# Kernel tuning notes

Hardware: AMD Instinct MI355X
Metric: run time of the kernel (lower is better)

## Reference

```python
import jax, jax.numpy as jnp
import numpy as np

B, H, A, D = 4096, 50, 32, 64          # batch, history len, neighbor count, embed_dim
NU, NV = 100000, 100000                # num users, num items
L = H + A                              # total gathered entries per node


def setup_inputs() -> dict:
    key = jax.random.key(0)
    ks = jax.random.split(key, 16)
    # embedding tables (u2e/v2e uniform(-1,1) as in module init, r2e ~ N(0,1) default)
    u2e = jax.random.uniform(ks[0], (NU, D), minval=-1.0, maxval=1.0, dtype=jnp.float32)
    v2e = jax.random.uniform(ks[1], (NV, D), minval=-1.0, maxval=1.0, dtype=jnp.float32)
    r2e = jax.random.normal(ks[2], (7, D), dtype=jnp.float32)
    relation_att = jax.random.normal(ks[3], (2 * D,), dtype=jnp.float32)
    s = 1.0 / np.sqrt(2 * D)  # torch Linear default init bound
    agg_W = jax.random.uniform(ks[4], (D, 2 * D), minval=-s, maxval=s, dtype=jnp.float32)
    agg_b = jax.random.uniform(ks[5], (D,), minval=-s, maxval=s, dtype=jnp.float32)
    lin1_W = jax.random.uniform(ks[6], (D, 2 * D), minval=-s, maxval=s, dtype=jnp.float32)
    lin1_b = jax.random.uniform(ks[7], (D,), minval=-s, maxval=s, dtype=jnp.float32)
    nodes_u = jax.random.randint(ks[8], (B,), 0, NU)
    nodes_v = jax.random.randint(ks[9], (B,), 0, NV)
    hist_u = jax.random.randint(ks[10], (B, H), 0, NV)   # user history = items
    hist_ur = jax.random.randint(ks[11], (B, H), 0, 6)   # ratings 0..5
    adj_u = jax.random.randint(ks[12], (B, A), 0, NU)    # social neighbors = users
    hist_v = jax.random.randint(ks[13], (B, H), 0, NU)   # item history = users
    hist_vr = jax.random.randint(ks[14], (B, H), 0, 6)
    adj_v = jax.random.randint(ks[15], (B, A), 0, NV)    # item-adj neighbors = items
    return dict(u2e=u2e, v2e=v2e, r2e=r2e, relation_att=relation_att,
                agg_W=agg_W, agg_b=agg_b, lin1_W=lin1_W, lin1_b=lin1_b,
                nodes_u=nodes_u, nodes_v=nodes_v,
                hist_u=hist_u, hist_ur=hist_ur, adj_u=adj_u,
                hist_v=hist_v, hist_vr=hist_vr, adj_v=adj_v)


def _encode(node_tab, target_tab, hist_tab, neigh_tab, r2e, relation_att,
            agg_W, agg_b, lin1_W, lin1_b, nodes, targets, hn, hr, adj):
    # Node_Encoder.forward + Node_Aggregator (percent=1.0 -> deterministic:
    # multinomial selects all indices; softmax-weighted sum is permutation-invariant).
    nf = node_tab[nodes]                                   # [B, D]
    tf = target_tab[targets]                               # [B, D]
    # query (computed as in original; with percent=1 the norm-softmax sampling
    # probability does not affect the output)
    _q = jnp.concatenate([nf, tf], axis=-1) @ agg_W.T + agg_b  # [B, D]
    hist_feat = jnp.concatenate([hist_tab[hn], neigh_tab[adj]], axis=1)  # [B, L, D]
    rates = jnp.concatenate([hr, jnp.full(adj.shape, 6, dtype=hr.dtype)], axis=1)
    rate_feat = r2e[rates]                                 # [B, L, D]
    sel = jnp.concatenate([hist_feat, rate_feat], axis=-1)  # [B, L, 2D]
    logits = jnp.einsum('ble,e->bl', sel, relation_att)    # [B, L]
    p = jax.nn.softmax(logits, axis=1)                     # softmax2 over entries
    neigh = jnp.einsum('bl,bld->bd', p, hist_feat)         # weighted sum [B, D]
    comb = jnp.concatenate([nf, neigh], axis=-1)           # [B, 2D]
    return jax.nn.relu(comb @ lin1_W.T + lin1_b)           # [B, D]


def reference(u2e, v2e, r2e, relation_att, agg_W, agg_b, lin1_W, lin1_b,
              nodes_u, nodes_v, hist_u, hist_ur, adj_u, hist_v, hist_vr, adj_v):
    # user side: isitem=False -> node=u2e, target=v2e, hist=v2e, neighbor=u2e
    eu = _encode(u2e, v2e, v2e, u2e, r2e, relation_att, agg_W, agg_b, lin1_W, lin1_b,
                 nodes_u, nodes_v, hist_u, hist_ur, adj_u)
    # item side: isitem=True -> node=v2e, target=u2e, hist=u2e, neighbor=v2e
    ev = _encode(v2e, u2e, u2e, v2e, r2e, relation_att, agg_W, agg_b, lin1_W, lin1_b,
                 nodes_v, nodes_u, hist_v, hist_vr, adj_v)
    return jnp.sum(eu * ev, axis=1)                        # [B]
```

## Files before the change

kernel.cpp:

```cpp
#include <hip/hip_runtime.h>


#define NB 4096
#define NH 50
#define NA 32
#define ND 64

__global__ __launch_bounds__(256, 4) void graphconsis_main(
    const float* __restrict__ u2e, const float* __restrict__ v2e,
    const float* __restrict__ r2e, const float* __restrict__ ra,
    const float* __restrict__ lin1_W, const float* __restrict__ lin1_b,
    const int* __restrict__ nodes_u, const int* __restrict__ nodes_v,
    const int* __restrict__ hist_u, const int* __restrict__ hist_ur,
    const int* __restrict__ adj_u,
    const int* __restrict__ hist_v, const int* __restrict__ hist_vr,
    const int* __restrict__ adj_v,
    float* __restrict__ out)
{
    __shared__ float lds_comb[4][128];
    __shared__ float ed[4][64];

    const int wid  = threadIdx.x >> 6;
    const int lane = threadIdx.x & 63;
    const int g    = lane >> 4;
    const int j    = lane & 15;
    const int side = wid >> 1;
    const int b    = __builtin_amdgcn_readfirstlane(blockIdx.x * 2 + (wid & 1));

    const float* nodeTab  = side ? v2e : u2e;
    const float* histTab  = side ? u2e : v2e;
    const float* neighTab = side ? v2e : u2e;
    const int* nodes = side ? nodes_v : nodes_u;
    const int* hn    = side ? hist_v  : hist_u;
    const int* hr    = side ? hist_vr : hist_ur;
    const int* adj   = side ? adj_v   : adj_u;

    const float4 ra4 = *(const float4*)(ra + 4 * j);

    const int lcl  = (lane < NH) ? lane : NH - 1;
    const int hraw = hn[b * NH + lcl];
    const int rraw = hr[b * NH + lcl];
    const int araw = adj[b * NA + (lane & 31)];

    int hidx[13];
    #pragma unroll
    for (int k = 0; k < 13; ++k) {
        int l = 4 * k + g; if (l > NH - 1) l = NH - 1;
        hidx[k] = __shfl(hraw, l);
    }
    int aidx[8];
    #pragma unroll
    for (int k = 0; k < 8; ++k)
        aidx[k] = __shfl(araw, 4 * k + g);
    const int hrv = __shfl(rraw, (4 * j + g < NH) ? (4 * j + g) : NH - 1);
    const bool hrv_valid = (4 * j + g) < NH;

    const float4 nf4 = *(const float4*)(nodeTab + nodes[b] * ND + 4 * j);
    float4 rh[13];
    #pragma unroll
    for (int k = 0; k < 13; ++k)
        rh[k] = *(const float4*)(histTab + hidx[k] * ND + 4 * j);
    float4 raj[8];
    #pragma unroll
    for (int k = 0; k < 8; ++k)
        raj[k] = *(const float4*)(neighTab + aidx[k] * ND + 4 * j);

    const float ra_hi = ra[64 + lane];
    float r0, r1, r2, r3, r4, r5, r6;
    {
        float t[7];
        #pragma unroll
        for (int r = 0; r < 7; ++r) {
            float part = r2e[r * 64 + lane] * ra_hi;
            part += __shfl_xor(part, 1);
            part += __shfl_xor(part, 2);
            part += __shfl_xor(part, 4);
            part += __shfl_xor(part, 8);
            part += __shfl_xor(part, 16);
            part += __shfl_xor(part, 32);
            t[r] = part;
        }
        r0 = t[0]; r1 = t[1]; r2 = t[2]; r3 = t[3]; r4 = t[4]; r5 = t[5]; r6 = t[6];
    }
    float rl0 = r6;
    rl0 = (hrv == 0) ? r0 : rl0;
    rl0 = (hrv == 1) ? r1 : rl0;
    rl0 = (hrv == 2) ? r2 : rl0;
    rl0 = (hrv == 3) ? r3 : rl0;
    rl0 = (hrv == 4) ? r4 : rl0;
    rl0 = (hrv == 5) ? r5 : rl0;
    rl0 = hrv_valid ? rl0 : r6;
    const float rlog6 = r6;

    float ssum = 0.f;
    float4 acc = make_float4(0.f, 0.f, 0.f, 0.f);

    #pragma unroll
    for (int k = 0; k < 12; ++k) {
        const float4 e = rh[k];
        float part = e.x * ra4.x;
        part = fmaf(e.y, ra4.y, part);
        part = fmaf(e.z, ra4.z, part);
        part = fmaf(e.w, ra4.w, part);
        part += (j == k) ? rl0 : 0.f;
        part += __shfl_xor(part, 1);
        part += __shfl_xor(part, 2);
        part += __shfl_xor(part, 4);
        part += __shfl_xor(part, 8);
        const float p = __expf(part);
        ssum += p;
        acc.x = fmaf(p, e.x, acc.x);
        acc.y = fmaf(p, e.y, acc.y);
        acc.z = fmaf(p, e.z, acc.z);
        acc.w = fmaf(p, e.w, acc.w);
    }
    {
        const float4 e = rh[12];
        float part = e.x * ra4.x;
        part = fmaf(e.y, ra4.y, part);
        part = fmaf(e.z, ra4.z, part);
        part = fmaf(e.w, ra4.w, part);
        part += (j == 12) ? rl0 : 0.f;
        part += __shfl_xor(part, 1);
        part += __shfl_xor(part, 2);
        part += __shfl_xor(part, 4);
        part += __shfl_xor(part, 8);
        const float p = (g < 2) ? __expf(part) : 0.f;
        ssum += p;
        acc.x = fmaf(p, e.x, acc.x);
        acc.y = fmaf(p, e.y, acc.y);
        acc.z = fmaf(p, e.z, acc.z);
        acc.w = fmaf(p, e.w, acc.w);
    }
    #pragma unroll
    for (int k = 0; k < 8; ++k) {
        const float4 e = raj[k];
        float part = e.x * ra4.x;
        part = fmaf(e.y, ra4.y, part);
        part = fmaf(e.z, ra4.z, part);
        part = fmaf(e.w, ra4.w, part);
        part += __shfl_xor(part, 1);
        part += __shfl_xor(part, 2);
        part += __shfl_xor(part, 4);
        part += __shfl_xor(part, 8);
        const float p = __expf(part + rlog6);
        ssum += p;
        acc.x = fmaf(p, e.x, acc.x);
        acc.y = fmaf(p, e.y, acc.y);
        acc.z = fmaf(p, e.z, acc.z);
        acc.w = fmaf(p, e.w, acc.w);
    }

    ssum += __shfl_xor(ssum, 16);
    ssum += __shfl_xor(ssum, 32);
    acc.x += __shfl_xor(acc.x, 16); acc.x += __shfl_xor(acc.x, 32);
    acc.y += __shfl_xor(acc.y, 16); acc.y += __shfl_xor(acc.y, 32);
    acc.z += __shfl_xor(acc.z, 16); acc.z += __shfl_xor(acc.z, 32);
    acc.w += __shfl_xor(acc.w, 16); acc.w += __shfl_xor(acc.w, 32);

    const float inv = 1.0f / ssum;

    if (g == 0) {
        *(float4*)&lds_comb[wid][4 * j] = nf4;
        float4 n4 = make_float4(acc.x * inv, acc.y * inv, acc.z * inv, acc.w * inv);
        *(float4*)&lds_comb[wid][64 + 4 * j] = n4;
    }

    float o = lin1_b[lane];
    const float4* W4 = (const float4*)(lin1_W + lane * 128);
    const float4* C4 = (const float4*)lds_comb[wid];
    #pragma unroll 8
    for (int kk = 0; kk < 32; ++kk) {
        const float4 w = W4[kk];
        const float4 c = C4[kk];
        o = fmaf(w.x, c.x, o);
        o = fmaf(w.y, c.y, o);
        o = fmaf(w.z, c.z, o);
        o = fmaf(w.w, c.w, o);
    }
    const float evec = fmaxf(o, 0.f);

    ed[wid][lane] = evec;
    __syncthreads();

    if (wid < 2) {
        float prod = ed[wid][lane] * ed[wid + 2][lane];
        #pragma unroll
        for (int off = 32; off >= 1; off >>= 1)
            prod += __shfl_xor(prod, off);
        if (lane == 0) out[blockIdx.x * 2 + wid] = prod;
    }
}

extern "C" void kernel_launch(void* const* d_in, const int* in_sizes, int n_in,
                              void* d_out, int out_size, void* d_ws, size_t ws_size,
                              hipStream_t stream)
{
    const float* u2e     = (const float*)d_in[0];
    const float* v2e     = (const float*)d_in[1];
    const float* r2e     = (const float*)d_in[2];
    const float* ra      = (const float*)d_in[3];
    const float* lin1_W  = (const float*)d_in[6];
    const float* lin1_b  = (const float*)d_in[7];
    const int* nodes_u   = (const int*)d_in[8];
    const int* nodes_v   = (const int*)d_in[9];
    const int* hist_u    = (const int*)d_in[10];
    const int* hist_ur   = (const int*)d_in[11];
    const int* adj_u     = (const int*)d_in[12];
    const int* hist_v    = (const int*)d_in[13];
    const int* hist_vr   = (const int*)d_in[14];
    const int* adj_v     = (const int*)d_in[15];
    float* out = (float*)d_out;

    hipLaunchKernelGGL(graphconsis_main, dim3(NB / 2), dim3(256), 0, stream,
                       u2e, v2e, r2e, ra, lin1_W, lin1_b,
                       nodes_u, nodes_v, hist_u, hist_ur, adj_u,
                       hist_v, hist_vr, adj_v, out);
}
```

Baseline: 59.60 us.

## Stream gathered embedding rows through LDS with async global_load_lds pipeline

Replaces the up-front register gather of all 21 embedding float4 rows per lane with a software pipeline. Each row is loaded asynchronously into per-wave LDS slots via global_load_lds, with 7 loads in flight and explicit vmcnt waits, and computation is interleaved with the loads. This cuts register pressure, which is why the occupancy hint was dropped from launch_bounds, and overlaps the r2e logit reduction with the loads. The cost is LDS usage (32KB per block), which limits occupancy, plus serialized waits. The node feature load is also moved after the aggregation loop.

```diff
diff --git a/kernel.cpp b/kernel.cpp
--- a/kernel.cpp
+++ b/kernel.cpp
@@ -5,8 +5,12 @@
 #define NH 50
 #define NA 32
 #define ND 64
-
-__global__ __launch_bounds__(256, 4) void graphconsis_main(
+#define SLOTS 8
+
+typedef const __attribute__((address_space(1))) unsigned int* gld_src_t;
+typedef __attribute__((address_space(3))) unsigned int* gld_dst_t;
+
+__global__ __launch_bounds__(256) void graphconsis_main(
     const float* __restrict__ u2e, const float* __restrict__ v2e,
     const float* __restrict__ r2e, const float* __restrict__ ra,
     const float* __restrict__ lin1_W, const float* __restrict__ lin1_b,
@@ -17,6 +21,7 @@
     const int* __restrict__ adj_v,
     float* __restrict__ out)
 {
+    __shared__ __align__(16) float stage[4][SLOTS][256];
     __shared__ float lds_comb[4][128];
     __shared__ float ed[4][64];
 
@@ -35,121 +40,98 @@
     const int* hr    = side ? hist_vr : hist_ur;
     const int* adj   = side ? adj_v   : adj_u;
 
-    const float4 ra4 = *(const float4*)(ra + 4 * j);
+    const float4 ra4  = *(const float4*)(ra + 4 * j);
+    const float ra_hi = ra[64 + lane];
 
     const int lcl  = (lane < NH) ? lane : NH - 1;
     const int hraw = hn[b * NH + lcl];
     const int rraw = hr[b * NH + lcl];
     const int araw = adj[b * NA + (lane & 31)];
 
-    int hidx[13];
+    float r2v[7];
+    #pragma unroll
+    for (int r = 0; r < 7; ++r) r2v[r] = r2e[r * 64 + lane];
+
+    int idx[21];
     #pragma unroll
     for (int k = 0; k < 13; ++k) {
         int l = 4 * k + g; if (l > NH - 1) l = NH - 1;
-        hidx[k] = __shfl(hraw, l);
-    }
-    int aidx[8];
+        idx[k] = __shfl(hraw, l);
+    }
     #pragma unroll
     for (int k = 0; k < 8; ++k)
-        aidx[k] = __shfl(araw, 4 * k + g);
+        idx[13 + k] = __shfl(araw, 4 * k + g);
+
     const int hrv = __shfl(rraw, (4 * j + g < NH) ? (4 * j + g) : NH - 1);
-    const bool hrv_valid = (4 * j + g) < NH;
-
-    const float4 nf4 = *(const float4*)(nodeTab + nodes[b] * ND + 4 * j);
-    float4 rh[13];
-    #pragma unroll
-    for (int k = 0; k < 13; ++k)
-        rh[k] = *(const float4*)(histTab + hidx[k] * ND + 4 * j);
-    float4 raj[8];
-    #pragma unroll
-    for (int k = 0; k < 8; ++k)
-        raj[k] = *(const float4*)(neighTab + aidx[k] * ND + 4 * j);
-
-    const float ra_hi = ra[64 + lane];
-    float r0, r1, r2, r3, r4, r5, r6;
-    {
-        float t[7];
-        #pragma unroll
-        for (int r = 0; r < 7; ++r) {
-            float part = r2e[r * 64 + lane] * ra_hi;
-            part += __shfl_xor(part, 1);
-            part += __shfl_xor(part, 2);
-            part += __shfl_xor(part, 4);
-            part += __shfl_xor(part, 8);
-            part += __shfl_xor(part, 16);
-            part += __shfl_xor(part, 32);
-            t[r] = part;
-        }
-        r0 = t[0]; r1 = t[1]; r2 = t[2]; r3 = t[3]; r4 = t[4]; r5 = t[5]; r6 = t[6];
-    }
-    float rl0 = r6;
-    rl0 = (hrv == 0) ? r0 : rl0;
-    rl0 = (hrv == 1) ? r1 : rl0;
-    rl0 = (hrv == 2) ? r2 : rl0;
-    rl0 = (hrv == 3) ? r3 : rl0;
-    rl0 = (hrv == 4) ? r4 : rl0;
-    rl0 = (hrv == 5) ? r5 : rl0;
-    rl0 = hrv_valid ? rl0 : r6;
-    const float rlog6 = r6;
-
-    float ssum = 0.f;
-    float4 acc = make_float4(0.f, 0.f, 0.f, 0.f);
-
-    #pragma unroll
-    for (int k = 0; k < 12; ++k) {
-        const float4 e = rh[k];
-        float part = e.x * ra4.x;
-        part = fmaf(e.y, ra4.y, part);
-        part = fmaf(e.z, ra4.z, part);
-        part = fmaf(e.w, ra4.w, part);
-        part += (j == k) ? rl0 : 0.f;
+
+    asm volatile("s_waitcnt vmcnt(0)" ::: "memory");
+
+#define ISSUE(k) do {                                                          \
+        const float* _s = (((k) < 13) ? histTab : neighTab)                    \
+                          + (size_t)idx[(k)] * ND + 4 * j;                     \
+        __builtin_amdgcn_global_load_lds((gld_src_t)(const void*)_s,           \
+            (gld_dst_t)(void*)&stage[wid][(k) % SLOTS][0], 16, 0, 0);          \
+    } while (0)
+
+    #pragma unroll
+    for (int k = 0; k < 7; ++k) ISSUE(k);
+
+    float t[7];
+    #pragma unroll
+    for (int r = 0; r < 7; ++r) {
+        float part = r2v[r] * ra_hi;
         part += __shfl_xor(part, 1);
         part += __shfl_xor(part, 2);
         part += __shfl_xor(part, 4);
         part += __shfl_xor(part, 8);
-        const float p = __expf(part);
-        ssum += p;
-        acc.x = fmaf(p, e.x, acc.x);
-        acc.y = fmaf(p, e.y, acc.y);
-        acc.z = fmaf(p, e.z, acc.z);
-        acc.w = fmaf(p, e.w, acc.w);
-    }
-    {
-        const float4 e = rh[12];
-        float part = e.x * ra4.x;
-        part = fmaf(e.y, ra4.y, part);
-        part = fmaf(e.z, ra4.z, part);
-        part = fmaf(e.w, ra4.w, part);
-        part += (j == 12) ? rl0 : 0.f;
-        part += __shfl_xor(part, 1);
-        part += __shfl_xor(part, 2);
-        part += __shfl_xor(part, 4);
-        part += __shfl_xor(part, 8);
-        const float p = (g < 2) ? __expf(part) : 0.f;
-        ssum += p;
-        acc.x = fmaf(p, e.x, acc.x);
-        acc.y = fmaf(p, e.y, acc.y);
-        acc.z = fmaf(p, e.z, acc.z);
-        acc.w = fmaf(p, e.w, acc.w);
-    }
-    #pragma unroll
-    for (int k = 0; k < 8; ++k) {
-        const float4 e = raj[k];
-        float part = e.x * ra4.x;
-        part = fmaf(e.y, ra4.y, part);
-        part = fmaf(e.z, ra4.z, part);
-        part = fmaf(e.w, ra4.w, part);
-        part += __shfl_xor(part, 1);
-        part += __shfl_xor(part, 2);
-        part += __shfl_xor(part, 4);
-        part += __shfl_xor(part, 8);
-        const float p = __expf(part + rlog6);
-        ssum += p;
-        acc.x = fmaf(p, e.x, acc.x);
-        acc.y = fmaf(p, e.y, acc.y);
-        acc.z = fmaf(p, e.z, acc.z);
-        acc.w = fmaf(p, e.w, acc.w);
-    }
+        part += __shfl_xor(part, 16);
+        part += __shfl_xor(part, 32);
+        t[r] = part;
+    }
+    float rl0 = t[6];
+    rl0 = (hrv == 0) ? t[0] : rl0;
+    rl0 = (hrv == 1) ? t[1] : rl0;
+    rl0 = (hrv == 2) ? t[2] : rl0;
+    rl0 = (hrv == 3) ? t[3] : rl0;
+    rl0 = (hrv == 4) ? t[4] : rl0;
+    rl0 = (hrv == 5) ? t[5] : rl0;
+    const float rlog6 = t[6];
+
+    float ssum = 0.f;
+    float4 acc = make_float4(0.f, 0.f, 0.f, 0.f);
+
+#define STEP(k, N) do {                                                        \
+        asm volatile("s_waitcnt lgkmcnt(0)" ::: "memory");                     \
+        if ((k) + 7 < 21) { ISSUE((k) + 7); }                                  \
+        asm volatile("s_waitcnt vmcnt(" #N ")" ::: "memory");                  \
+        const float4 e = *(const float4*)&stage[wid][(k) % SLOTS][lane * 4];   \
+        float part = e.x * ra4.x;                                              \
+        part = fmaf(e.y, ra4.y, part);                                         \
+        part = fmaf(e.z, ra4.z, part);                                         \
+        part = fmaf(e.w, ra4.w, part);                                         \
+        if ((k) < 13) part += (j == (k)) ? rl0 : 0.f;                          \
+        part += __shfl_xor(part, 1);                                           \
+        part += __shfl_xor(part, 2);                                           \
+        part += __shfl_xor(part, 4);                                           \
+        part += __shfl_xor(part, 8);                                           \
+        if ((k) >= 13) part += rlog6;                                          \
+        float p = __expf(part);                                                \
+        if ((k) == 12) { if (g >= 2) p = 0.f; }                                \
+        ssum += p;                                                             \
+        acc.x = fmaf(p, e.x, acc.x);                                           \
+        acc.y = fmaf(p, e.y, acc.y);                                           \
+        acc.z = fmaf(p, e.z, acc.z);                                           \
+        acc.w = fmaf(p, e.w, acc.w);                                           \
+    } while (0);
+
+    STEP(0, 7)  STEP(1, 7)  STEP(2, 7)  STEP(3, 7)  STEP(4, 7)
+    STEP(5, 7)  STEP(6, 7)  STEP(7, 7)  STEP(8, 7)  STEP(9, 7)
+    STEP(10, 7) STEP(11, 7) STEP(12, 7) STEP(13, 7)
+    STEP(14, 6) STEP(15, 5) STEP(16, 4) STEP(17, 3)
+    STEP(18, 2) STEP(19, 1) STEP(20, 0)
+
+#undef STEP
+#undef ISSUE
 
     ssum += __shfl_xor(ssum, 16);
     ssum += __shfl_xor(ssum, 32);
@@ -159,6 +141,8 @@
     acc.w += __shfl_xor(acc.w, 16); acc.w += __shfl_xor(acc.w, 32);
 
     const float inv = 1.0f / ssum;
+
+    const float4 nf4 = *(const float4*)(nodeTab + nodes[b] * ND + 4 * j);
 
     if (g == 0) {
         *(float4*)&lds_comb[wid][4 * j] = nf4;
```

Result: faster. 56.32 us (median of 2 runs) (-5.5%).
